# Kernel tuning notes

Hardware: AMD Instinct MI355X
Metric: run time of the kernel (lower is better)

The kernel has to match this reference:

```python
import jax, jax.numpy as jnp
import numpy as np

V, E, H, N, L = 32000, 512, 512, 64, 128


def setup_inputs() -> dict:
    key = jax.random.key(0)
    ks = jax.random.split(key, 16)
    s = 0.02  # init scale
    return {
        "input_ids": jax.random.randint(ks[0], (N,), 0, V),
        "h": jax.random.normal(ks[1], (N, H), jnp.float32),
        "c": jax.random.normal(ks[2], (N, H), jnp.float32),
        "encoder_hiddens": jax.random.normal(ks[3], (N, L, H), jnp.float32),
        "attn_mask": jnp.zeros((N, L), dtype=bool),
        "embed_W": jax.random.normal(ks[4], (V, E), jnp.float32) * s,
        "w_ih": jax.random.normal(ks[5], (4 * H, E), jnp.float32) * s,
        "b_ih": jnp.zeros((4 * H,), jnp.float32),
        "w_hh": jax.random.normal(ks[6], (4 * H, H), jnp.float32) * s,
        "b_hh": jnp.zeros((4 * H,), jnp.float32),
        "attn_Wh": jax.random.normal(ks[7], (H, H), jnp.float32) * s,
        "attn_Ws": jax.random.normal(ks[8], (H, H), jnp.float32) * s,
        "attn_v": jax.random.normal(ks[9], (H,), jnp.float32) * s,
        "h2o_W": jax.random.normal(ks[10], (V, 2 * H), jnp.float32) * s,
        "h2o_b": jnp.zeros((V,), jnp.float32),
    }


def reference(input_ids, h, c, encoder_hiddens, attn_mask, embed_W,
              w_ih, b_ih, w_hh, b_hh, attn_Wh, attn_Ws, attn_v,
              h2o_W, h2o_b):
    # Embedding lookup: (N, E)
    emb = embed_W[input_ids]
    # LSTM cell: fused gate GEMMs, chunk order i, f, g, o (torch chunk(4))
    gates = emb @ w_ih.T + b_ih + h @ w_hh.T + b_hh  # (N, 4H)
    i_g, f_g, g_g, o_g = jnp.split(gates, 4, axis=1)
    c_t = jax.nn.sigmoid(f_g) * c + jax.nn.sigmoid(i_g) * jnp.tanh(g_g)
    h_t = jax.nn.sigmoid(o_g) * jnp.tanh(c_t)  # (N, H)
    # Bahdanau attention: v^T tanh(W_h h_t + W_s enc)
    proj = jnp.tanh((h_t @ attn_Wh.T)[:, None, :] + encoder_hiddens @ attn_Ws.T)  # (N, L, H)
    score = jnp.einsum('nlh,h->nl', proj, attn_v)  # (N, L)
    score = jnp.where(attn_mask, -jnp.inf, score)
    attn_w = jax.nn.softmax(score, axis=1)  # (N, L)
    context = jnp.einsum('nl,nlh->nh', attn_w, encoder_hiddens)  # (N, H)
    # Output projection + log-softmax over vocab
    combined = jnp.concatenate([h_t, context], axis=1)  # (N, 2H)
    out = jax.nn.log_softmax(combined @ h2o_W.T + h2o_b, axis=-1)  # (N, V)
    return out, h_t, c_t
```

## Files before the change

kernel.cpp:

```cpp
#include <hip/hip_runtime.h>
#include <hip/hip_bf16.h>
#include <math.h>

#define V 32000
#define E 512
#define H 512
#define N 64
#define L 128
#define NV (N*V)
#define NH (N*H)
#define MTOT (N*L)
#define VT 500

typedef short  s8v  __attribute__((ext_vector_type(8)));
typedef float  f4v  __attribute__((ext_vector_type(4)));

__device__ __forceinline__ float sigf(float x) { return 1.0f / (1.0f + __expf(-x)); }

__device__ __forceinline__ unsigned short f2bf(float f) {
    unsigned int u = __float_as_uint(f);
    unsigned int r = u + 0x7FFFu + ((u >> 16) & 1u);
    return (unsigned short)(r >> 16);
}

__device__ __forceinline__ unsigned int cvt2bf(float x, float y) {
    __hip_bfloat162 h2 = __float22bfloat162_rn(make_float2(x, y));
    unsigned int r;
    __builtin_memcpy(&r, &h2, 4);
    return r;
}

__device__ __forceinline__ uint4 pack_q(float4 lo, float4 hi) {
    uint4 q;
    q.x = cvt2bf(lo.x, lo.y); q.y = cvt2bf(lo.z, lo.w);
    q.z = cvt2bf(hi.x, hi.y); q.w = cvt2bf(hi.z, hi.w);
    return q;
}

__global__ __launch_bounds__(256) void k_gates(
    const int* __restrict__ ids, const float* __restrict__ hprev,
    const float* __restrict__ embW, const float* __restrict__ w_ih,
    const float* __restrict__ w_hh, float* __restrict__ gates_p)
{
    __shared__ __align__(16) float xs[64 * 128];
    const int bx = blockIdx.x;
    const int ks = blockIdx.y;
    const int tid = threadIdx.x;
    const bool emb_part = (ks < 4);
    const int koff = (ks & 3) * 128;

    for (int i = tid; i < 64 * 32; i += 256) {
        int n = i >> 5, kk4 = i & 31;
        float4 x4;
        if (emb_part)
            x4 = ((const float4*)(embW + (size_t)ids[n] * E + koff))[kk4];
        else
            x4 = ((const float4*)(hprev + (size_t)n * H + koff))[kk4];
        ((float4*)xs)[n * 32 + kk4] = x4;
    }
    __syncthreads();

    const int jl = tid & 63;
    const int ng = tid >> 6;
    const int j = bx * 64 + jl;
    const int nb = ng * 16;
    const float* wrow = (emb_part ? w_ih : w_hh) + (size_t)j * 512 + koff;

    float acc[16];
#pragma unroll
    for (int i = 0; i < 16; ++i) acc[i] = 0.f;

    for (int e4 = 0; e4 < 32; ++e4) {
        float4 w4 = ((const float4*)wrow)[e4];
#pragma unroll
        for (int i = 0; i < 16; ++i) {
            float4 x4 = ((const float4*)xs)[(nb + i) * 32 + e4];
            acc[i] += w4.x * x4.x + w4.y * x4.y + w4.z * x4.z + w4.w * x4.w;
        }
    }
#pragma unroll
    for (int i = 0; i < 16; ++i)
        gates_p[(size_t)ks * (64 * 2048) + (size_t)(nb + i) * 2048 + j] = acc[i];
}

__global__ __launch_bounds__(256) void k_lstm_pw(
    const float* __restrict__ gates_p, const float* __restrict__ b_ih,
    const float* __restrict__ b_hh, const float* __restrict__ cprev,
    float* __restrict__ out, unsigned short* __restrict__ xb)
{
    int i = blockIdx.x * 256 + threadIdx.x;
    if (i >= NH) return;
    int n = i >> 9, k = i & 511;
    float g[4];
#pragma unroll
    for (int q = 0; q < 4; ++q) {
        int j = q * 512 + k;
        float s = b_ih[j] + b_hh[j];
#pragma unroll
        for (int ks = 0; ks < 8; ++ks)
            s += gates_p[(size_t)ks * (64 * 2048) + (size_t)n * 2048 + j];
        g[q] = s;
    }
    float ig = sigf(g[0]), fg = sigf(g[1]), gg = tanhf(g[2]), og = sigf(g[3]);
    float ct = fg * cprev[i] + ig * gg;
    float ht = og * tanhf(ct);
    out[NV + i] = ht;
    out[NV + NH + i] = ct;
    xb[(size_t)n * 1024 + k] = f2bf(ht);
}

__global__ __launch_bounds__(256) void k_sproj(
    const float* __restrict__ out, const float* __restrict__ Wh,
    float* __restrict__ sproj)
{
    __shared__ __align__(16) float xs[512];
    int n = blockIdx.x >> 1;
    int h = (blockIdx.x & 1) * 256 + threadIdx.x;
    const float* ht = out + NV + (size_t)n * 512;
    for (int i = threadIdx.x; i < 512; i += 256) xs[i] = ht[i];
    __syncthreads();
    const float* wrow = Wh + (size_t)h * 512;
    float acc = 0.f;
    for (int e4 = 0; e4 < 128; ++e4) {
        float4 w4 = ((const float4*)wrow)[e4];
        float4 x4 = ((const float4*)xs)[e4];
        acc += w4.x * x4.x + w4.y * x4.y + w4.z * x4.z + w4.w * x4.w;
    }
    sproj[(size_t)n * 512 + h] = acc;
}

__global__ __launch_bounds__(256) void k_score_gemm(
    const float* __restrict__ enc, const float* __restrict__ Ws,
    const float* __restrict__ sproj, const float* __restrict__ av,
    float* __restrict__ scorep)
{
    __shared__ __align__(16) short As[64 * 72];
    __shared__ __align__(16) short Bs[64 * 72];
    __shared__ float sred[64];

    const int bm = blockIdx.x, bh = blockIdx.y;
    const int tid = threadIdx.x;
    const int w = tid >> 6, l = tid & 63;
    const int wave_m = (w >> 1) * 32, wave_h = (w & 1) * 32;
    const int lq = l >> 4, lr = l & 15;

    if (tid < 64) sred[tid] = 0.f;

    f4v acc[2][2];
#pragma unroll
    for (int i = 0; i < 2; ++i)
#pragma unroll
        for (int j = 0; j < 2; ++j) acc[i][j] = (f4v)0.f;

    for (int kt = 0; kt < 8; ++kt) {
        __syncthreads();
#pragma unroll
        for (int r = 0; r < 2; ++r) {
            int idx = (r * 256 + tid) * 8;
            int row = idx >> 6, col = idx & 63;
            const float* sa = enc + (size_t)(bm * 64 + row) * 512 + kt * 64 + col;
            const float* sb = Ws  + (size_t)(bh * 64 + row) * 512 + kt * 64 + col;
            float4 a0 = *(const float4*)sa, a1 = *(const float4*)(sa + 4);
            float4 b0 = *(const float4*)sb, b1 = *(const float4*)(sb + 4);
            *(uint4*)(As + row * 72 + col) = pack_q(a0, a1);
            *(uint4*)(Bs + row * 72 + col) = pack_q(b0, b1);
        }
        __syncthreads();

#pragma unroll
        for (int ks = 0; ks < 2; ++ks) {
            s8v a_frag[2], b_frag[2];
#pragma unroll
            for (int i = 0; i < 2; ++i)
                a_frag[i] = *(const s8v*)(As + (wave_m + 16 * i + lr) * 72 + ks * 32 + lq * 8);
#pragma unroll
            for (int j = 0; j < 2; ++j)
                b_frag[j] = *(const s8v*)(Bs + (wave_h + 16 * j + lr) * 72 + ks * 32 + lq * 8);
#pragma unroll
            for (int i = 0; i < 2; ++i)
#pragma unroll
                for (int j = 0; j < 2; ++j)
                    acc[i][j] = __builtin_amdgcn_mfma_f32_16x16x32_bf16(
                        a_frag[i], b_frag[j], acc[i][j], 0, 0, 0);
        }
    }
    __syncthreads();

    const int hc0 = bh * 64 + wave_h + lr;
#pragma unroll
    for (int i = 0; i < 2; ++i) {
#pragma unroll
        for (int reg = 0; reg < 4; ++reg) {
            int m_local = wave_m + 16 * i + lq * 4 + reg;
            int m = bm * 64 + m_local;
            int n = m >> 7;
            float p = 0.f;
#pragma unroll
            for (int j = 0; j < 2; ++j) {
                int hc = hc0 + 16 * j;
                float val = acc[i][j][reg] + sproj[(size_t)n * 512 + hc];
                p += tanhf(val) * av[hc];
            }
            p += __shfl_xor(p, 1, 64);
            p += __shfl_xor(p, 2, 64);
            p += __shfl_xor(p, 4, 64);
            p += __shfl_xor(p, 8, 64);
            if (lr == 0) atomicAdd(&sred[m_local], p);
        }
    }
    __syncthreads();
    if (tid < 64)
        scorep[(size_t)bh * MTOT + bm * 64 + tid] = sred[tid];
}

__global__ __launch_bounds__(128) void k_softmax_ctx(
    const float* __restrict__ scorep, const unsigned char* __restrict__ mask,
    const float* __restrict__ enc, unsigned short* __restrict__ xb)
{
    __shared__ float wl[128];
    __shared__ float red[4];
    const int n = blockIdx.x, hc = blockIdx.y, t = threadIdx.x;

    float s = 0.f;
#pragma unroll
    for (int q = 0; q < 8; ++q)
        s += scorep[(size_t)q * MTOT + n * 128 + t];
    if (mask[(size_t)n * 128 + t]) s = -1e30f;

    float m = s;
#pragma unroll
    for (int off = 32; off > 0; off >>= 1) m = fmaxf(m, __shfl_xor(m, off, 64));
    if ((t & 63) == 0) red[t >> 6] = m;
    __syncthreads();
    m = fmaxf(red[0], red[1]);
    float e = __expf(s - m);
    float ss = e;
#pragma unroll
    for (int off = 32; off > 0; off >>= 1) ss += __shfl_xor(ss, off, 64);
    if ((t & 63) == 0) red[2 + (t >> 6)] = ss;
    __syncthreads();
    float inv = 1.0f / (red[2] + red[3]);
    wl[t] = e * inv;
    __syncthreads();

    const float* encn = enc + (size_t)n * (L * H) + hc * 128 + t;
    float acc = 0.f;
#pragma unroll 8
    for (int ll = 0; ll < 128; ++ll)
        acc += wl[ll] * encn[(size_t)ll * 512];
    xb[(size_t)n * 1024 + 512 + hc * 128 + t] = f2bf(acc);
}

__global__ __launch_bounds__(512) void k_logits(
    const float* __restrict__ h2oW, const unsigned short* __restrict__ xb,
    const float* __restrict__ h2ob, float* __restrict__ dlogits,
    float* __restrict__ pmax, float* __restrict__ psum)
{
    __shared__ __align__(16) short As[2][64 * 72];
    __shared__ __align__(16) short Bs[2][64 * 72];
    __shared__ __align__(16) float cs[64 * 68];

    const int bm = blockIdx.x;
    const int tid = threadIdx.x;
    const int g = tid >> 8;
    const int tl = tid & 255;
    const int w2 = (tid >> 6) & 3;
    const int l = tid & 63;
    const int wave_m = (w2 & 1) * 32, wave_n = (w2 >> 1) * 32;
    const int lq = l >> 4, lr = l & 15;

    const int arow = tl >> 2;
    const int acol = (tl & 3) * 16;
    const float* aptr = h2oW + (size_t)(bm * 64 + arow) * 1024 + g * 512 + acol;
    const unsigned short* bptr = xb + (size_t)arow * 1024 + g * 512 + acol;

    short* Asg = As[g];
    short* Bsg = Bs[g];

    f4v acc[2][2];
#pragma unroll
    for (int i = 0; i < 2; ++i)
#pragma unroll
        for (int j = 0; j < 2; ++j) acc[i][j] = (f4v)0.f;

#pragma unroll 1
    for (int kt = 0; kt < 8; ++kt) {
        if (kt) __syncthreads();
        const float* ap = aptr + kt * 64;
        const unsigned short* bp = bptr + kt * 64;
        float4 a0 = ((const float4*)ap)[0], a1 = ((const float4*)ap)[1];
        float4 a2 = ((const float4*)ap)[2], a3 = ((const float4*)ap)[3];
        uint4 b0 = *(const uint4*)bp, b1 = *(const uint4*)(bp + 8);
        *(uint4*)(Asg + arow * 72 + acol)     = pack_q(a0, a1);
        *(uint4*)(Asg + arow * 72 + acol + 8) = pack_q(a2, a3);
        *(uint4*)(Bsg + arow * 72 + acol)     = b0;
        *(uint4*)(Bsg + arow * 72 + acol + 8) = b1;
        __syncthreads();

#pragma unroll
        for (int ks = 0; ks < 2; ++ks) {
            s8v a_frag[2], b_frag[2];
#pragma unroll
            for (int i = 0; i < 2; ++i)
                a_frag[i] = *(const s8v*)(Asg + (wave_m + 16 * i + lr) * 72 + ks * 32 + lq * 8);
#pragma unroll
            for (int j = 0; j < 2; ++j)
                b_frag[j] = *(const s8v*)(Bsg + (wave_n + 16 * j + lr) * 72 + ks * 32 + lq * 8);
#pragma unroll
            for (int i = 0; i < 2; ++i)
#pragma unroll
                for (int j = 0; j < 2; ++j)
                    acc[i][j] = __builtin_amdgcn_mfma_f32_16x16x32_bf16(
                        a_frag[i], b_frag[j], acc[i][j], 0, 0, 0);
        }
    }
    __syncthreads();

    if (g == 0) {
#pragma unroll
        for (int i = 0; i < 2; ++i)
#pragma unroll
            for (int j = 0; j < 2; ++j)
#pragma unroll
                for (int reg = 0; reg < 4; ++reg)
                    cs[(wave_n + 16 * j + lr) * 68 + wave_m + 16 * i + lq * 4 + reg] = acc[i][j][reg];
    }
    __syncthreads();
    if (g == 1) {
#pragma unroll
        for (int i = 0; i < 2; ++i)
#pragma unroll
            for (int j = 0; j < 2; ++j)
#pragma unroll
                for (int reg = 0; reg < 4; ++reg)
                    cs[(wave_n + 16 * j + lr) * 68 + wave_m + 16 * i + lq * 4 + reg] += acc[i][j][reg];
    }
    __syncthreads();

    if (tid < 256) {
        const int n = tid >> 2, q = tid & 3;
        const int v0 = bm * 64 + q * 16;
        float4 vals[4];
        float m_loc = -1e30f;
#pragma unroll
        for (int k = 0; k < 4; ++k) {
            float4 cv = *(const float4*)(cs + n * 68 + q * 16 + 4 * k);
            float4 bv = *(const float4*)(h2ob + v0 + 4 * k);
            cv.x += bv.x; cv.y += bv.y; cv.z += bv.z; cv.w += bv.w;
            vals[k] = cv;
            *(float4*)(dlogits + (size_t)n * V + v0 + 4 * k) = cv;
            m_loc = fmaxf(m_loc, fmaxf(fmaxf(cv.x, cv.y), fmaxf(cv.z, cv.w)));
        }
        float s_loc = 0.f;
#pragma unroll
        for (int k = 0; k < 4; ++k) {
            s_loc += __expf(vals[k].x - m_loc) + __expf(vals[k].y - m_loc)
                   + __expf(vals[k].z - m_loc) + __expf(vals[k].w - m_loc);
        }
        float m2 = fmaxf(m_loc, __shfl_xor(m_loc, 1, 64));
        m2 = fmaxf(m2, __shfl_xor(m2, 2, 64));
        s_loc *= __expf(m_loc - m2);
        float s2 = s_loc + __shfl_xor(s_loc, 1, 64);
        s2 += __shfl_xor(s2, 2, 64);
        if (q == 0) {
            pmax[(size_t)n * VT + bm] = m2;
            psum[(size_t)n * VT + bm] = s2;
        }
    }
}

__global__ __launch_bounds__(256) void k_lse_norm(
    const float* __restrict__ pmax, const float* __restrict__ psum,
    float* __restrict__ dlogits)
{
    __shared__ float rm[4], rs[4];
    __shared__ float lsev;
    const int n = blockIdx.x, ch = blockIdx.y, t = threadIdx.x;
    float m0 = (t < VT) ? pmax[(size_t)n * VT + t] : -1e30f;
    float m1 = (t + 256 < VT) ? pmax[(size_t)n * VT + t + 256] : -1e30f;
    float mm = fmaxf(m0, m1);
#pragma unroll
    for (int off = 32; off > 0; off >>= 1) mm = fmaxf(mm, __shfl_xor(mm, off, 64));
    if ((t & 63) == 0) rm[t >> 6] = mm;
    __syncthreads();
    float m = fmaxf(fmaxf(rm[0], rm[1]), fmaxf(rm[2], rm[3]));

    float s = 0.f;
    if (t < VT)       s += psum[(size_t)n * VT + t] * __expf(m0 - m);
    if (t + 256 < VT) s += psum[(size_t)n * VT + t + 256] * __expf(m1 - m);
#pragma unroll
    for (int off = 32; off > 0; off >>= 1) s += __shfl_xor(s, off, 64);
    if ((t & 63) == 0) rs[t >> 6] = s;
    __syncthreads();
    if (t == 0) {
        float st = rs[0] + rs[1] + rs[2] + rs[3];
        lsev = m + __logf(st);
    }
    __syncthreads();
    const float lse = lsev;

    float4* row = (float4*)(dlogits + (size_t)n * V) + ch * 1000;
#pragma unroll 2
    for (int idx = t; idx < 1000; idx += 256) {
        float4 v = row[idx];
        v.x -= lse; v.y -= lse; v.z -= lse; v.w -= lse;
        row[idx] = v;
    }
}

extern "C" void kernel_launch(void* const* d_in, const int* in_sizes, int n_in,
                              void* d_out, int out_size, void* d_ws, size_t ws_size,
                              hipStream_t stream)
{
    const int* ids   = (const int*)d_in[0];
    const float* h   = (const float*)d_in[1];
    const float* c   = (const float*)d_in[2];
    const float* enc = (const float*)d_in[3];
    const unsigned char* mask = (const unsigned char*)d_in[4];
    const float* embW = (const float*)d_in[5];
    const float* w_ih = (const float*)d_in[6];
    const float* b_ih = (const float*)d_in[7];
    const float* w_hh = (const float*)d_in[8];
    const float* b_hh = (const float*)d_in[9];
    const float* Wh   = (const float*)d_in[10];
    const float* Ws   = (const float*)d_in[11];
    const float* av   = (const float*)d_in[12];
    const float* h2oW = (const float*)d_in[13];
    const float* h2ob = (const float*)d_in[14];

    float* out = (float*)d_out;
    float* ws = (float*)d_ws;
    float* gates_p = ws;
    float* sproj   = ws + 1048576;
    float* scorep  = ws + 1048576 + 32768;
    unsigned short* xb = (unsigned short*)(ws + 1048576 + 32768 + 65536);
    float* pmax = ws;
    float* psum = ws + 32000;

    k_gates<<<dim3(32, 8), 256, 0, stream>>>(ids, h, embW, w_ih, w_hh, gates_p);
    k_lstm_pw<<<128, 256, 0, stream>>>(gates_p, b_ih, b_hh, c, out, xb);
    k_sproj<<<128, 256, 0, stream>>>(out, Wh, sproj);
    k_score_gemm<<<dim3(128, 8), 256, 0, stream>>>(enc, Ws, sproj, av, scorep);
    k_softmax_ctx<<<dim3(64, 4), 128, 0, stream>>>(scorep, mask, enc, xb);
    k_logits<<<VT, 512, 0, stream>>>(h2oW, xb, h2ob, out, pmax, psum);
    k_lse_norm<<<dim3(64, 8), 256, 0, stream>>>(pmax, psum, out);
}
```

Baseline: 334.5 us.

## Fold h_t·Wh projection into score GEMM as extra K phase, drop k_sproj

Removes the separate k_sproj kernel. The score GEMM now runs a second 8-step K loop that multiplies the bf16 h_t (read from xb and broadcast across all 64 rows of the M tile) against Wh, so the accumulator already holds W_h h + W_s enc before tanh. This saves one launch and the sproj round-trip through memory, but repeats the h·Wh work for every M tile, doubling MFMA and B-load work in the score kernel. It also computes that projection in bf16 instead of fp32. Separately, k_gates moves to 512 threads with 8 rows per thread, and k_lstm_pw moves to 128-thread blocks.

After: 323.3 us, median of 2. 1.03x faster.

```diff
diff --git a/kernel.cpp b/kernel.cpp
--- a/kernel.cpp
+++ b/kernel.cpp
@@ -37,7 +37,7 @@
     return q;
 }
 
-__global__ __launch_bounds__(256) void k_gates(
+__global__ __launch_bounds__(512) void k_gates(
     const int* __restrict__ ids, const float* __restrict__ hprev,
     const float* __restrict__ embW, const float* __restrict__ w_ih,
     const float* __restrict__ w_hh, float* __restrict__ gates_p)
@@ -49,7 +49,7 @@
     const bool emb_part = (ks < 4);
     const int koff = (ks & 3) * 128;
 
-    for (int i = tid; i < 64 * 32; i += 256) {
+    for (int i = tid; i < 64 * 32; i += 512) {
         int n = i >> 5, kk4 = i & 31;
         float4 x4;
         if (emb_part)
@@ -63,32 +63,32 @@
     const int jl = tid & 63;
     const int ng = tid >> 6;
     const int j = bx * 64 + jl;
-    const int nb = ng * 16;
+    const int nb = ng * 8;
     const float* wrow = (emb_part ? w_ih : w_hh) + (size_t)j * 512 + koff;
 
-    float acc[16];
-#pragma unroll
-    for (int i = 0; i < 16; ++i) acc[i] = 0.f;
+    float acc[8];
+#pragma unroll
+    for (int i = 0; i < 8; ++i) acc[i] = 0.f;
 
     for (int e4 = 0; e4 < 32; ++e4) {
         float4 w4 = ((const float4*)wrow)[e4];
 #pragma unroll
-        for (int i = 0; i < 16; ++i) {
+        for (int i = 0; i < 8; ++i) {
             float4 x4 = ((const float4*)xs)[(nb + i) * 32 + e4];
             acc[i] += w4.x * x4.x + w4.y * x4.y + w4.z * x4.z + w4.w * x4.w;
         }
     }
 #pragma unroll
-    for (int i = 0; i < 16; ++i)
+    for (int i = 0; i < 8; ++i)
         gates_p[(size_t)ks * (64 * 2048) + (size_t)(nb + i) * 2048 + j] = acc[i];
 }
 
-__global__ __launch_bounds__(256) void k_lstm_pw(
+__global__ __launch_bounds__(128) void k_lstm_pw(
     const float* __restrict__ gates_p, const float* __restrict__ b_ih,
     const float* __restrict__ b_hh, const float* __restrict__ cprev,
     float* __restrict__ out, unsigned short* __restrict__ xb)
 {
-    int i = blockIdx.x * 256 + threadIdx.x;
+    int i = blockIdx.x * 128 + threadIdx.x;
     if (i >= NH) return;
     int n = i >> 9, k = i & 511;
     float g[4];
@@ -109,30 +109,10 @@
     xb[(size_t)n * 1024 + k] = f2bf(ht);
 }
 
-__global__ __launch_bounds__(256) void k_sproj(
-    const float* __restrict__ out, const float* __restrict__ Wh,
-    float* __restrict__ sproj)
-{
-    __shared__ __align__(16) float xs[512];
-    int n = blockIdx.x >> 1;
-    int h = (blockIdx.x & 1) * 256 + threadIdx.x;
-    const float* ht = out + NV + (size_t)n * 512;
-    for (int i = threadIdx.x; i < 512; i += 256) xs[i] = ht[i];
-    __syncthreads();
-    const float* wrow = Wh + (size_t)h * 512;
-    float acc = 0.f;
-    for (int e4 = 0; e4 < 128; ++e4) {
-        float4 w4 = ((const float4*)wrow)[e4];
-        float4 x4 = ((const float4*)xs)[e4];
-        acc += w4.x * x4.x + w4.y * x4.y + w4.z * x4.z + w4.w * x4.w;
-    }
-    sproj[(size_t)n * 512 + h] = acc;
-}
-
 __global__ __launch_bounds__(256) void k_score_gemm(
     const float* __restrict__ enc, const float* __restrict__ Ws,
-    const float* __restrict__ sproj, const float* __restrict__ av,
-    float* __restrict__ scorep)
+    const float* __restrict__ Wh, const unsigned short* __restrict__ xb,
+    const float* __restrict__ av, float* __restrict__ scorep)
 {
     __shared__ __align__(16) short As[64 * 72];
     __shared__ __align__(16) short Bs[64 * 72];
@@ -143,6 +123,7 @@
     const int w = tid >> 6, l = tid & 63;
     const int wave_m = (w >> 1) * 32, wave_h = (w & 1) * 32;
     const int lq = l >> 4, lr = l & 15;
+    const int n = bm >> 1;
 
     if (tid < 64) sred[tid] = 0.f;
 
@@ -151,6 +132,26 @@
     for (int i = 0; i < 2; ++i)
 #pragma unroll
         for (int j = 0; j < 2; ++j) acc[i][j] = (f4v)0.f;
+
+#define MFMA_PHASE()                                                       \
+    {                                                                      \
+        _Pragma("unroll")                                                  \
+        for (int ks = 0; ks < 2; ++ks) {                                   \
+            s8v a_frag[2], b_frag[2];                                      \
+            _Pragma("unroll")                                              \
+            for (int i = 0; i < 2; ++i)                                    \
+                a_frag[i] = *(const s8v*)(As + (wave_m + 16 * i + lr) * 72 + ks * 32 + lq * 8); \
+            _Pragma("unroll")                                              \
+            for (int j = 0; j < 2; ++j)                                    \
+                b_frag[j] = *(const s8v*)(Bs + (wave_h + 16 * j + lr) * 72 + ks * 32 + lq * 8); \
+            _Pragma("unroll")                                              \
+            for (int i = 0; i < 2; ++i)                                    \
+                _Pragma("unroll")                                          \
+                for (int j = 0; j < 2; ++j)                                \
+                    acc[i][j] = __builtin_amdgcn_mfma_f32_16x16x32_bf16(   \
+                        a_frag[i], b_frag[j], acc[i][j], 0, 0, 0);         \
+        }                                                                  \
+    }
 
     for (int kt = 0; kt < 8; ++kt) {
         __syncthreads();
@@ -166,24 +167,25 @@
             *(uint4*)(Bs + row * 72 + col) = pack_q(b0, b1);
         }
         __syncthreads();
-
-#pragma unroll
-        for (int ks = 0; ks < 2; ++ks) {
-            s8v a_frag[2], b_frag[2];
-#pragma unroll
-            for (int i = 0; i < 2; ++i)
-                a_frag[i] = *(const s8v*)(As + (wave_m + 16 * i + lr) * 72 + ks * 32 + lq * 8);
-#pragma unroll
-            for (int j = 0; j < 2; ++j)
-                b_frag[j] = *(const s8v*)(Bs + (wave_h + 16 * j + lr) * 72 + ks * 32 + lq * 8);
-#pragma unroll
-            for (int i = 0; i < 2; ++i)
-#pragma unroll
-                for (int j = 0; j < 2; ++j)
-                    acc[i][j] = __builtin_amdgcn_mfma_f32_16x16x32_bf16(
-                        a_frag[i], b_frag[j], acc[i][j], 0, 0, 0);
-        }
-    }
+        MFMA_PHASE();
+    }
+
+    for (int kt = 0; kt < 8; ++kt) {
+        __syncthreads();
+#pragma unroll
+        for (int r = 0; r < 2; ++r) {
+            int idx = (r * 256 + tid) * 8;
+            int row = idx >> 6, col = idx & 63;
+            uint4 ha = *(const uint4*)(xb + (size_t)n * 1024 + kt * 64 + col);
+            const float* sb = Wh + (size_t)(bh * 64 + row) * 512 + kt * 64 + col;
+            float4 b0 = *(const float4*)sb, b1 = *(const float4*)(sb + 4);
+            *(uint4*)(As + row * 72 + col) = ha;
+            *(uint4*)(Bs + row * 72 + col) = pack_q(b0, b1);
+        }
+        __syncthreads();
+        MFMA_PHASE();
+    }
+#undef MFMA_PHASE
     __syncthreads();
 
     const int hc0 = bh * 64 + wave_h + lr;
@@ -192,14 +194,11 @@
 #pragma unroll
         for (int reg = 0; reg < 4; ++reg) {
             int m_local = wave_m + 16 * i + lq * 4 + reg;
-            int m = bm * 64 + m_local;
-            int n = m >> 7;
             float p = 0.f;
 #pragma unroll
             for (int j = 0; j < 2; ++j) {
                 int hc = hc0 + 16 * j;
-                float val = acc[i][j][reg] + sproj[(size_t)n * 512 + hc];
-                p += tanhf(val) * av[hc];
+                p += tanhf(acc[i][j][reg]) * av[hc];
             }
             p += __shfl_xor(p, 1, 64);
             p += __shfl_xor(p, 2, 64);
@@ -431,16 +430,14 @@
     float* out = (float*)d_out;
     float* ws = (float*)d_ws;
     float* gates_p = ws;
-    float* sproj   = ws + 1048576;
     float* scorep  = ws + 1048576 + 32768;
     unsigned short* xb = (unsigned short*)(ws + 1048576 + 32768 + 65536);
     float* pmax = ws;
     float* psum = ws + 32000;
 
-    k_gates<<<dim3(32, 8), 256, 0, stream>>>(ids, h, embW, w_ih, w_hh, gates_p);
-    k_lstm_pw<<<128, 256, 0, stream>>>(gates_p, b_ih, b_hh, c, out, xb);
-    k_sproj<<<128, 256, 0, stream>>>(out, Wh, sproj);
-    k_score_gemm<<<dim3(128, 8), 256, 0, stream>>>(enc, Ws, sproj, av, scorep);
+    k_gates<<<dim3(32, 8), 512, 0, stream>>>(ids, h, embW, w_ih, w_hh, gates_p);
+    k_lstm_pw<<<256, 128, 0, stream>>>(gates_p, b_ih, b_hh, c, out, xb);
+    k_score_gemm<<<dim3(128, 8), 256, 0, stream>>>(enc, Ws, Wh, xb, av, scorep);
     k_softmax_ctx<<<dim3(64, 4), 128, 0, stream>>>(scorep, mask, enc, xb);
     k_logits<<<VT, 512, 0, stream>>>(h2oW, xb, h2ob, out, pmax, psum);
     k_lse_norm<<<dim3(64, 8), 256, 0, stream>>>(pmax, psum, out);
```
